# Performance work log

Measured on AMD Instinct MI355X. Metric: run time of the kernel, lower is better.

Reference implementation:

```python
import jax, jax.numpy as jnp
import numpy as np

N = 1024       # gaussians
H = 256
W = 256
C = 64         # spectral channels
K = 2          # gabor components per gaussian
RADIUS_CLIP = 1.0
CHOL_BOUND = np.array([0.5, 0.0, 0.5], dtype=np.float32)


def setup_inputs() -> dict:
    key = jax.random.key(0)
    k1, k2, k3, k4, k5 = jax.random.split(key, 5)
    # _xyz = atanh(2*(rand-0.5))
    u = jax.random.uniform(k1, (N, 2), minval=-0.999, maxval=0.999)
    xyz = jnp.arctanh(u)
    cholesky = jax.random.uniform(k2, (N, 3))
    opacity = jnp.ones((N, 1), dtype=jnp.float32)
    # features init: inverse_softplus(0.05) + 0.01*randn
    inv_sp = float(np.log(np.expm1(0.05)))
    features_dc = inv_sp + 0.01 * jax.random.normal(k3, (N, C))
    gabor_freqs = (jax.random.uniform(k4, (N * K, 2)) - 0.5) * 0.002
    gabor_weights = jax.random.uniform(k5, (N * K, 1)) * -5.0
    return {
        'xyz': xyz, 'cholesky': cholesky, 'opacity': opacity,
        'features_dc': features_dc, 'gabor_freqs': gabor_freqs,
        'gabor_weights': gabor_weights,
    }


def _render(xyz, cholesky, opacity, features_dc, gabor_freqs, gabor_weights):
    # --- project_gaussians_2d ---
    xy = jnp.tanh(xyz)                              # [N,2] in (-1,1)
    xs = 0.5 * W * (xy[:, 0] + 1.0)                 # pixel-space centers
    ys = 0.5 * H * (xy[:, 1] + 1.0)
    L = cholesky + jnp.asarray(CHOL_BOUND)[None, :]  # [N,3] -> l1,l2,l3
    l1, l2, l3 = L[:, 0], L[:, 1], L[:, 2]
    # Sigma = L L^T, L = [[l1,0],[l2,l3]]
    s11 = l1 * l1
    s12 = l1 * l2
    s22 = l2 * l2 + l3 * l3
    det = (l1 * l3) ** 2
    ca = s22 / det                                  # conic = Sigma^-1
    cb = -s12 / det
    cc = s11 / det
    # radius = ceil(3*sqrt(max eigenvalue)); prune tiny gaussians
    mid = 0.5 * (s11 + s22)
    lam_max = mid + jnp.sqrt(jnp.maximum(mid * mid - det, 1e-8))
    radius = jnp.ceil(3.0 * jnp.sqrt(lam_max))
    keep = (radius > RADIUS_CLIP).astype(xyz.dtype)  # [N]

    # --- rasterize_gabor_sum (dense reference; kernel tiles, math identical) ---
    px = jnp.arange(W, dtype=xyz.dtype) + 0.5
    py = jnp.arange(H, dtype=xyz.dtype) + 0.5
    pxf = jnp.tile(px, H)                            # [HW]
    pyf = jnp.repeat(py, W)                          # [HW]
    dx = xs[:, None] - pxf[None, :]                  # [N,HW]
    dy = ys[:, None] - pyf[None, :]
    sigma = 0.5 * (ca[:, None] * dx * dx + cc[:, None] * dy * dy) + cb[:, None] * dx * dy
    alpha = opacity * jnp.exp(-sigma) * keep[:, None]  # [N,HW]

    freqs = jnp.exp(gabor_freqs).reshape(N, K, 2)
    wts = jax.nn.sigmoid(gabor_weights).reshape(N, K)
    mod = jnp.ones_like(dx)
    for k in range(K):  # K=2, structurally small loop
        mod = mod + wts[:, k, None] * jnp.cos(freqs[:, k, 0, None] * dx + freqs[:, k, 1, None] * dy)

    wmap = alpha * mod                               # [N,HW]
    feats = jax.nn.softplus(features_dc)             # [N,C]
    out = jnp.einsum('np,nc->pc', wmap, feats)       # [HW,C], sum compositing
    out = jnp.clip(out, 0.0, 1.0)
    return out.reshape(1, H, W, C).transpose(0, 3, 1, 2)  # [1,C,H,W]


def reference(xyz, cholesky, opacity, features_dc, gabor_freqs, gabor_weights):
    return _render(xyz, cholesky, opacity, features_dc, gabor_freqs, gabor_weights)
```

## Files before the change

### kernel.cpp

```cpp
#include <hip/hip_runtime.h>
#include <hip/hip_bf16.h>

#define NG     1024
#define NC     64
#define CULL_T 15.0f
#define MAXL   256
#define KPAD   72
#define L2E    1.44269504f
#define INV2PI 0.15915494f

typedef float    f32x4 __attribute__((ext_vector_type(4)));
typedef _Float16 f16x4 __attribute__((ext_vector_type(4)));
typedef _Float16 f16x2 __attribute__((ext_vector_type(2)));

__device__ __forceinline__ float wgt_f(float4 p0, float4 p1, float4 p2,
                                       float pxf, float pyf) {
    const float dx = p0.x - pxf, dy = p0.y - pyf;
    const float t  = fmaf(p0.w, dy, p0.z * dx);
    const float s2 = fmaf(p1.x * dy, dy, dx * t);
    const float e  = __builtin_amdgcn_exp2f(s2);
    const float r1 = fmaf(p2.x, dx, p2.y * dy);
    const float c1 = __builtin_amdgcn_cosf(__builtin_amdgcn_fractf(r1));
    const float r2 = fmaf(p2.z, dx, p2.w * dy);
    const float c2 = __builtin_amdgcn_cosf(__builtin_amdgcn_fractf(r2));
    const float m  = fmaf(p1.w, c2, fmaf(p1.z, c1, 1.f));
    return e * p1.y * m;
}

__global__ __launch_bounds__(512) void fused_mfma_kernel(
    const float* __restrict__ xyz,  const float* __restrict__ chol,
    const float* __restrict__ opac, const float* __restrict__ fdc,
    const float* __restrict__ gfrq, const float* __restrict__ gwts,
    float* __restrict__ out)
{
    __shared__ float4 s_p0[MAXL], s_p1[MAXL], s_p2[MAXL];
    __shared__ unsigned short s_list[MAXL];
    __shared__ int s_scnt[16];
    __shared__ _Float16 A_lds[NC][KPAD];
    __shared__ _Float16 B_lds[256][KPAD];

    const int tid  = threadIdx.x;
    const int lane = tid & 63, w = tid >> 6;

    const int x0 = (blockIdx.x & 7) << 5;
    const int y0 = (blockIdx.x >> 3) << 3;
    const float xlo = x0 + 0.5f, xhi = x0 + 31.5f;
    const float ylo = y0 + 0.5f, yhi = y0 + 7.5f;

    float4 P0[2], P1[2], P2[2];
    bool   lv[2];
    int    pos[2];
    #pragma unroll
    for (int r = 0; r < 2; ++r) {
        const int n = (r << 9) + tid;
        const float2 xy = ((const float2*)xyz)[n];
        const float ex = __builtin_amdgcn_exp2f(2.f * L2E * xy.x);
        const float ey = __builtin_amdgcn_exp2f(2.f * L2E * xy.y);
        const float xs = 256.f - 256.f * __builtin_amdgcn_rcpf(1.f + ex);
        const float ys = 256.f - 256.f * __builtin_amdgcn_rcpf(1.f + ey);

        const float l1 = chol[3*n]     + 0.5f;
        const float l2 = chol[3*n + 1];
        const float l3 = chol[3*n + 2] + 0.5f;
        const float s11 = l1*l1, s12 = l1*l2, s22 = l2*l2 + l3*l3;
        const float dt  = (l1*l3) * (l1*l3);
        const float inv = __builtin_amdgcn_rcpf(dt);
        const float na = -0.5f * L2E * s22 * inv;
        const float nb =          L2E * s12 * inv;
        const float nc = -0.5f * L2E * s11 * inv;
        const float mid = 0.5f * (s11 + s22);
        const float lam = mid + __builtin_amdgcn_sqrtf(fmaxf(mid*mid - dt, 1e-8f));
        const float radius = ceilf(3.f * __builtin_amdgcn_sqrtf(lam));
        const float keep = (radius > 1.0f) ? 1.f : 0.f;
        const float oK = opac[n] * keep;
        const float r2 = (oK != 0.f) ? (2.f * CULL_T * lam) : -1.f;

        const float nx = fminf(fmaxf(xs, xlo), xhi);
        const float ny = fminf(fmaxf(ys, ylo), yhi);
        const float ddx = xs - nx, ddy = ys - ny;
        lv[r] = (ddx*ddx + ddy*ddy) <= r2;

        const unsigned long long m = __ballot(lv[r]);
        pos[r] = __popcll(m & ((1ull << lane) - 1ull));
        if (lane == 0) s_scnt[(r << 3) + w] = __popcll(m);

        const float4 gf = ((const float4*)gfrq)[n];
        const float2 gw = ((const float2*)gwts)[n];
        P0[r] = make_float4(xs, ys, na, nb);
        P1[r] = make_float4(nc, oK,
            __builtin_amdgcn_rcpf(1.f + __builtin_amdgcn_exp2f(-L2E*gw.x)),
            __builtin_amdgcn_rcpf(1.f + __builtin_amdgcn_exp2f(-L2E*gw.y)));
        P2[r] = make_float4(
            __builtin_amdgcn_exp2f(L2E*gf.x)*INV2PI,
            __builtin_amdgcn_exp2f(L2E*gf.y)*INV2PI,
            __builtin_amdgcn_exp2f(L2E*gf.z)*INV2PI,
            __builtin_amdgcn_exp2f(L2E*gf.w)*INV2PI);
    }
    __syncthreads();

    int pre[17];
    pre[0] = 0;
    #pragma unroll
    for (int s = 0; s < 16; ++s) pre[s+1] = pre[s] + s_scnt[s];
    const int total = min(pre[16], MAXL);

    #pragma unroll
    for (int r = 0; r < 2; ++r) {
        if (lv[r]) {
            const int p = pre[(r << 3) + w] + pos[r];
            if (p < MAXL) {
                s_list[p] = (unsigned short)((r << 9) + tid);
                s_p0[p] = P0[r]; s_p1[p] = P1[r]; s_p2[p] = P2[r];
            }
        }
    }
    for (int idx = total + tid; idx < MAXL; idx += 512) {
        s_p0[idx] = make_float4(0,0,0,0);
        s_p1[idx] = make_float4(0,0,0,0);
        s_p2[idx] = make_float4(0,0,0,0);
    }
    __syncthreads();

    const int c15 = lane & 15, g = lane >> 4;

    f32x4 acc[4][2];
    #pragma unroll
    for (int a = 0; a < 4; ++a) {
        acc[a][0] = (f32x4){0.f,0.f,0.f,0.f};
        acc[a][1] = (f32x4){0.f,0.f,0.f,0.f};
    }

    float pxf[4], pyf[4];
    #pragma unroll
    for (int j = 0; j < 4; ++j) {
        const int px = j*64 + lane;
        pxf[j] = x0 + (px & 31) + 0.5f;
        pyf[j] = y0 + (px >> 5) + 0.5f;
    }

    for (int base = 0; base < total; base += 64) {
        const int rem = min(total - base, 64);
        const int nw  = (rem + 15) >> 4;

        {
            const int c = tid & 63, kq = tid >> 6;
            for (int i = 0; i < nw; ++i) {
                const int k0 = i*16 + kq*2;
                float v0 = 0.f, v1 = 0.f;
                if (k0 < rem) {
                    const int n = (int)s_list[base + k0];
                    const float x = fdc[(n << 6) + c];
                    v0 = 0.69314718f * __builtin_amdgcn_logf(
                             1.f + __builtin_amdgcn_exp2f(L2E * x));
                }
                if (k0 + 1 < rem) {
                    const int n = (int)s_list[base + k0 + 1];
                    const float x = fdc[(n << 6) + c];
                    v1 = 0.69314718f * __builtin_amdgcn_logf(
                             1.f + __builtin_amdgcn_exp2f(L2E * x));
                }
                *(f16x2*)&A_lds[c][k0] = (f16x2){(_Float16)v0, (_Float16)v1};
            }
        }

        for (int i = 0; i < nw; ++i) {
            const int k0 = 2*(i*8 + w);
            const float4 p0a = s_p0[base+k0],   p1a = s_p1[base+k0],   p2a = s_p2[base+k0];
            const float4 p0b = s_p0[base+k0+1], p1b = s_p1[base+k0+1], p2b = s_p2[base+k0+1];
            #pragma unroll
            for (int j = 0; j < 4; ++j) {
                const float w0 = wgt_f(p0a, p1a, p2a, pxf[j], pyf[j]);
                const float w1 = wgt_f(p0b, p1b, p2b, pxf[j], pyf[j]);
                const int px = j*64 + lane;
                *(f16x2*)&B_lds[px][k0] = (f16x2){(_Float16)w0, (_Float16)w1};
            }
        }
        __syncthreads();

        for (int kc = 0; kc < nw; ++kc) {
            const int kb = kc*16 + g*4;
            f16x4 af0 = *(const f16x4*)&A_lds[ 0 + c15][kb];
            f16x4 af1 = *(const f16x4*)&A_lds[16 + c15][kb];
            f16x4 af2 = *(const f16x4*)&A_lds[32 + c15][kb];
            f16x4 af3 = *(const f16x4*)&A_lds[48 + c15][kb];
            f16x4 bf0 = *(const f16x4*)&B_lds[(w*2+0)*16 + c15][kb];
            f16x4 bf1 = *(const f16x4*)&B_lds[(w*2+1)*16 + c15][kb];

            acc[0][0] = __builtin_amdgcn_mfma_f32_16x16x16f16(af0, bf0, acc[0][0], 0,0,0);
            acc[0][1] = __builtin_amdgcn_mfma_f32_16x16x16f16(af0, bf1, acc[0][1], 0,0,0);
            acc[1][0] = __builtin_amdgcn_mfma_f32_16x16x16f16(af1, bf0, acc[1][0], 0,0,0);
            acc[1][1] = __builtin_amdgcn_mfma_f32_16x16x16f16(af1, bf1, acc[1][1], 0,0,0);
            acc[2][0] = __builtin_amdgcn_mfma_f32_16x16x16f16(af2, bf0, acc[2][0], 0,0,0);
            acc[2][1] = __builtin_amdgcn_mfma_f32_16x16x16f16(af2, bf1, acc[2][1], 0,0,0);
            acc[3][0] = __builtin_amdgcn_mfma_f32_16x16x16f16(af3, bf0, acc[3][0], 0,0,0);
            acc[3][1] = __builtin_amdgcn_mfma_f32_16x16x16f16(af3, bf1, acc[3][1], 0,0,0);
        }
        if (base + 64 < total) __syncthreads();
    }

    #pragma unroll
    for (int mt = 0; mt < 4; ++mt) {
        #pragma unroll
        for (int ntl = 0; ntl < 2; ++ntl) {
            const int px = (w*2 + ntl)*16 + c15;
            const int pg = ((y0 + (px >> 5)) << 8) + x0 + (px & 31);
            #pragma unroll
            for (int q = 0; q < 4; ++q) {
                const int ch = mt*16 + g*4 + q;
                out[(ch << 16) + pg] = fminf(fmaxf(acc[mt][ntl][q], 0.f), 1.f);
            }
        }
    }
}

extern "C" void kernel_launch(void* const* d_in, const int* in_sizes, int n_in,
                              void* d_out, int out_size, void* d_ws, size_t ws_size,
                              hipStream_t stream) {
    const float* xyz  = (const float*)d_in[0];
    const float* chol = (const float*)d_in[1];
    const float* opac = (const float*)d_in[2];
    const float* fdc  = (const float*)d_in[3];
    const float* gfrq = (const float*)d_in[4];
    const float* gwts = (const float*)d_in[5];

    fused_mfma_kernel<<<256, 512, 0, stream>>>(xyz, chol, opac, fdc,
                                               gfrq, gwts, (float*)d_out);
}
```

Baseline: 12.94 us.

## Compute Gabor weights directly into MFMA B registers, skip B LDS staging

Each lane now evaluates the Gaussian-Gabor weights it needs straight into the f16x4 B fragment, so the B_lds staging buffer and the per-chunk barriers go away. The softplus feature matrix A is built once for the whole culled list in a padded LDS array, and the Gabor parameters are loaded and transformed only for surviving Gaussians. Output stores become nontemporal. Per-lane transcendental work is unchanged in total, but the LDS traffic and synchronisation are removed in exchange for more registers per lane.

```diff
diff --git a/kernel.cpp b/kernel.cpp
--- a/kernel.cpp
+++ b/kernel.cpp
@@ -5,7 +5,7 @@
 #define NC     64
 #define CULL_T 15.0f
 #define MAXL   256
-#define KPAD   72
+#define APAD   258
 #define L2E    1.44269504f
 #define INV2PI 0.15915494f
 
@@ -36,8 +36,7 @@
     __shared__ float4 s_p0[MAXL], s_p1[MAXL], s_p2[MAXL];
     __shared__ unsigned short s_list[MAXL];
     __shared__ int s_scnt[16];
-    __shared__ _Float16 A_lds[NC][KPAD];
-    __shared__ _Float16 B_lds[256][KPAD];
+    __shared__ _Float16 A_lds[NC][APAD];
 
     const int tid  = threadIdx.x;
     const int lane = tid & 63, w = tid >> 6;
@@ -47,7 +46,8 @@
     const float xlo = x0 + 0.5f, xhi = x0 + 31.5f;
     const float ylo = y0 + 0.5f, yhi = y0 + 7.5f;
 
-    float4 P0[2], P1[2], P2[2];
+    float4 P0[2];
+    float  NCC[2], OK[2];
     bool   lv[2];
     int    pos[2];
     #pragma unroll
@@ -84,17 +84,8 @@
         pos[r] = __popcll(m & ((1ull << lane) - 1ull));
         if (lane == 0) s_scnt[(r << 3) + w] = __popcll(m);
 
-        const float4 gf = ((const float4*)gfrq)[n];
-        const float2 gw = ((const float2*)gwts)[n];
         P0[r] = make_float4(xs, ys, na, nb);
-        P1[r] = make_float4(nc, oK,
-            __builtin_amdgcn_rcpf(1.f + __builtin_amdgcn_exp2f(-L2E*gw.x)),
-            __builtin_amdgcn_rcpf(1.f + __builtin_amdgcn_exp2f(-L2E*gw.y)));
-        P2[r] = make_float4(
-            __builtin_amdgcn_exp2f(L2E*gf.x)*INV2PI,
-            __builtin_amdgcn_exp2f(L2E*gf.y)*INV2PI,
-            __builtin_amdgcn_exp2f(L2E*gf.z)*INV2PI,
-            __builtin_amdgcn_exp2f(L2E*gf.w)*INV2PI);
+        NCC[r] = nc; OK[r] = oK;
     }
     __syncthreads();
 
@@ -109,8 +100,19 @@
         if (lv[r]) {
             const int p = pre[(r << 3) + w] + pos[r];
             if (p < MAXL) {
-                s_list[p] = (unsigned short)((r << 9) + tid);
-                s_p0[p] = P0[r]; s_p1[p] = P1[r]; s_p2[p] = P2[r];
+                const int n = (r << 9) + tid;
+                const float4 gf = ((const float4*)gfrq)[n];
+                const float2 gw = ((const float2*)gwts)[n];
+                s_list[p] = (unsigned short)n;
+                s_p0[p] = P0[r];
+                s_p1[p] = make_float4(NCC[r], OK[r],
+                    __builtin_amdgcn_rcpf(1.f + __builtin_amdgcn_exp2f(-L2E*gw.x)),
+                    __builtin_amdgcn_rcpf(1.f + __builtin_amdgcn_exp2f(-L2E*gw.y)));
+                s_p2[p] = make_float4(
+                    __builtin_amdgcn_exp2f(L2E*gf.x)*INV2PI,
+                    __builtin_amdgcn_exp2f(L2E*gf.y)*INV2PI,
+                    __builtin_amdgcn_exp2f(L2E*gf.z)*INV2PI,
+                    __builtin_amdgcn_exp2f(L2E*gf.w)*INV2PI);
             }
         }
     }
@@ -121,7 +123,34 @@
     }
     __syncthreads();
 
+    const int nkc = (total + 15) >> 4;
+
+    {
+        const int c = tid & 63, kq = tid >> 6;
+        for (int i = 0; i < nkc; ++i) {
+            const int k0 = (i << 4) + (kq << 1);
+            float v0 = 0.f, v1 = 0.f;
+            if (k0 < total) {
+                const int n = (int)s_list[k0];
+                const float x = fdc[(n << 6) + c];
+                v0 = 0.69314718f * __builtin_amdgcn_logf(
+                         1.f + __builtin_amdgcn_exp2f(L2E * x));
+            }
+            if (k0 + 1 < total) {
+                const int n = (int)s_list[k0 + 1];
+                const float x = fdc[(n << 6) + c];
+                v1 = 0.69314718f * __builtin_amdgcn_logf(
+                         1.f + __builtin_amdgcn_exp2f(L2E * x));
+            }
+            *(f16x2*)&A_lds[c][k0] = (f16x2){(_Float16)v0, (_Float16)v1};
+        }
+    }
+    __syncthreads();
+
     const int c15 = lane & 15, g = lane >> 4;
+    const float pxf0 = x0 + c15 + 0.5f;
+    const float pxf1 = x0 + 16 + c15 + 0.5f;
+    const float pyf  = y0 + w + 0.5f;
 
     f32x4 acc[4][2];
     #pragma unroll
@@ -130,85 +159,50 @@
         acc[a][1] = (f32x4){0.f,0.f,0.f,0.f};
     }
 
-    float pxf[4], pyf[4];
-    #pragma unroll
-    for (int j = 0; j < 4; ++j) {
-        const int px = j*64 + lane;
-        pxf[j] = x0 + (px & 31) + 0.5f;
-        pyf[j] = y0 + (px >> 5) + 0.5f;
-    }
-
-    for (int base = 0; base < total; base += 64) {
-        const int rem = min(total - base, 64);
-        const int nw  = (rem + 15) >> 4;
-
-        {
-            const int c = tid & 63, kq = tid >> 6;
-            for (int i = 0; i < nw; ++i) {
-                const int k0 = i*16 + kq*2;
-                float v0 = 0.f, v1 = 0.f;
-                if (k0 < rem) {
-                    const int n = (int)s_list[base + k0];
-                    const float x = fdc[(n << 6) + c];
-                    v0 = 0.69314718f * __builtin_amdgcn_logf(
-                             1.f + __builtin_amdgcn_exp2f(L2E * x));
-                }
-                if (k0 + 1 < rem) {
-                    const int n = (int)s_list[base + k0 + 1];
-                    const float x = fdc[(n << 6) + c];
-                    v1 = 0.69314718f * __builtin_amdgcn_logf(
-                             1.f + __builtin_amdgcn_exp2f(L2E * x));
-                }
-                *(f16x2*)&A_lds[c][k0] = (f16x2){(_Float16)v0, (_Float16)v1};
-            }
-        }
-
-        for (int i = 0; i < nw; ++i) {
-            const int k0 = 2*(i*8 + w);
-            const float4 p0a = s_p0[base+k0],   p1a = s_p1[base+k0],   p2a = s_p2[base+k0];
-            const float4 p0b = s_p0[base+k0+1], p1b = s_p1[base+k0+1], p2b = s_p2[base+k0+1];
-            #pragma unroll
-            for (int j = 0; j < 4; ++j) {
-                const float w0 = wgt_f(p0a, p1a, p2a, pxf[j], pyf[j]);
-                const float w1 = wgt_f(p0b, p1b, p2b, pxf[j], pyf[j]);
-                const int px = j*64 + lane;
-                *(f16x2*)&B_lds[px][k0] = (f16x2){(_Float16)w0, (_Float16)w1};
-            }
-        }
-        __syncthreads();
-
-        for (int kc = 0; kc < nw; ++kc) {
-            const int kb = kc*16 + g*4;
-            f16x4 af0 = *(const f16x4*)&A_lds[ 0 + c15][kb];
-            f16x4 af1 = *(const f16x4*)&A_lds[16 + c15][kb];
-            f16x4 af2 = *(const f16x4*)&A_lds[32 + c15][kb];
-            f16x4 af3 = *(const f16x4*)&A_lds[48 + c15][kb];
-            f16x4 bf0 = *(const f16x4*)&B_lds[(w*2+0)*16 + c15][kb];
-            f16x4 bf1 = *(const f16x4*)&B_lds[(w*2+1)*16 + c15][kb];
-
-            acc[0][0] = __builtin_amdgcn_mfma_f32_16x16x16f16(af0, bf0, acc[0][0], 0,0,0);
-            acc[0][1] = __builtin_amdgcn_mfma_f32_16x16x16f16(af0, bf1, acc[0][1], 0,0,0);
-            acc[1][0] = __builtin_amdgcn_mfma_f32_16x16x16f16(af1, bf0, acc[1][0], 0,0,0);
-            acc[1][1] = __builtin_amdgcn_mfma_f32_16x16x16f16(af1, bf1, acc[1][1], 0,0,0);
-            acc[2][0] = __builtin_amdgcn_mfma_f32_16x16x16f16(af2, bf0, acc[2][0], 0,0,0);
-            acc[2][1] = __builtin_amdgcn_mfma_f32_16x16x16f16(af2, bf1, acc[2][1], 0,0,0);
-            acc[3][0] = __builtin_amdgcn_mfma_f32_16x16x16f16(af3, bf0, acc[3][0], 0,0,0);
-            acc[3][1] = __builtin_amdgcn_mfma_f32_16x16x16f16(af3, bf1, acc[3][1], 0,0,0);
-        }
-        if (base + 64 < total) __syncthreads();
-    }
-
+    for (int kc = 0; kc < nkc; ++kc) {
+        const int kb = (kc << 4) + (g << 2);
+
+        const float4 q00 = s_p0[kb],   q10 = s_p1[kb],   q20 = s_p2[kb];
+        const float4 q01 = s_p0[kb+1], q11 = s_p1[kb+1], q21 = s_p2[kb+1];
+        const float4 q02 = s_p0[kb+2], q12 = s_p1[kb+2], q22 = s_p2[kb+2];
+        const float4 q03 = s_p0[kb+3], q13 = s_p1[kb+3], q23 = s_p2[kb+3];
+
+        const f16x4 bf0 = {
+            (_Float16)wgt_f(q00, q10, q20, pxf0, pyf),
+            (_Float16)wgt_f(q01, q11, q21, pxf0, pyf),
+            (_Float16)wgt_f(q02, q12, q22, pxf0, pyf),
+            (_Float16)wgt_f(q03, q13, q23, pxf0, pyf) };
+        const f16x4 bf1 = {
+            (_Float16)wgt_f(q00, q10, q20, pxf1, pyf),
+            (_Float16)wgt_f(q01, q11, q21, pxf1, pyf),
+            (_Float16)wgt_f(q02, q12, q22, pxf1, pyf),
+            (_Float16)wgt_f(q03, q13, q23, pxf1, pyf) };
+
+        const f16x4 af0 = *(const f16x4*)&A_lds[ 0 + c15][kb];
+        const f16x4 af1 = *(const f16x4*)&A_lds[16 + c15][kb];
+        const f16x4 af2 = *(const f16x4*)&A_lds[32 + c15][kb];
+        const f16x4 af3 = *(const f16x4*)&A_lds[48 + c15][kb];
+
+        acc[0][0] = __builtin_amdgcn_mfma_f32_16x16x16f16(af0, bf0, acc[0][0], 0,0,0);
+        acc[0][1] = __builtin_amdgcn_mfma_f32_16x16x16f16(af0, bf1, acc[0][1], 0,0,0);
+        acc[1][0] = __builtin_amdgcn_mfma_f32_16x16x16f16(af1, bf0, acc[1][0], 0,0,0);
+        acc[1][1] = __builtin_amdgcn_mfma_f32_16x16x16f16(af1, bf1, acc[1][1], 0,0,0);
+        acc[2][0] = __builtin_amdgcn_mfma_f32_16x16x16f16(af2, bf0, acc[2][0], 0,0,0);
+        acc[2][1] = __builtin_amdgcn_mfma_f32_16x16x16f16(af2, bf1, acc[2][1], 0,0,0);
+        acc[3][0] = __builtin_amdgcn_mfma_f32_16x16x16f16(af3, bf0, acc[3][0], 0,0,0);
+        acc[3][1] = __builtin_amdgcn_mfma_f32_16x16x16f16(af3, bf1, acc[3][1], 0,0,0);
+    }
+
+    const int pg0 = ((y0 + w) << 8) + x0 + c15;
     #pragma unroll
     for (int mt = 0; mt < 4; ++mt) {
         #pragma unroll
-        for (int ntl = 0; ntl < 2; ++ntl) {
-            const int px = (w*2 + ntl)*16 + c15;
-            const int pg = ((y0 + (px >> 5)) << 8) + x0 + (px & 31);
-            #pragma unroll
-            for (int q = 0; q < 4; ++q) {
-                const int ch = mt*16 + g*4 + q;
-                out[(ch << 16) + pg] = fminf(fmaxf(acc[mt][ntl][q], 0.f), 1.f);
-            }
+        for (int q = 0; q < 4; ++q) {
+            const int ch = mt*16 + g*4 + q;
+            __builtin_nontemporal_store(
+                fminf(fmaxf(acc[mt][0][q], 0.f), 1.f), &out[(ch << 16) + pg0]);
+            __builtin_nontemporal_store(
+                fminf(fmaxf(acc[mt][1][q], 0.f), 1.f), &out[(ch << 16) + pg0 + 16]);
         }
     }
 }
```

Result: faster. 12.03 us (-7.0%).
